# Optimization experiments

Hardware: AMD Instinct MI355X
Metric: run time of the kernel (lower is better)

Reference implementation:

```python
import jax, jax.numpy as jnp
import numpy as np

ALPHA = 4.0   # spikingjelly surrogate.Sigmoid default
TAU = 2.0
VTH = 1.0
EPS = 1e-5

@jax.custom_vjp
def spike(x):
    return (x >= 0.0).astype(x.dtype)

def _spike_fwd(x):
    return spike(x), x

def _spike_bwd(x, g):
    s = jax.nn.sigmoid(ALPHA * x)
    return (g * ALPHA * s * (1.0 - s),)

spike.defvjp(_spike_fwd, _spike_bwd)

def lif(x):
    # x: [T, B, N, C]; multi-step LIF, v_reset=0 hard reset, detach_reset=True
    def step(v, xt):
        v = v + (xt - v) / TAU          # charge
        s = spike(v - VTH)              # fire (surrogate grad)
        v = v * (1.0 - jax.lax.stop_gradient(s))  # hard reset, detached
        return v, s
    _, out = jax.lax.scan(step, jnp.zeros_like(x[0]), x)
    return out

def bn(x, gamma, beta):
    # BatchNorm1d in training mode: per-channel (last dim) over all other dims
    mu = x.mean(axis=(0, 1, 2), keepdims=True)
    var = x.var(axis=(0, 1, 2), keepdims=True)  # biased var, as torch BN uses for normalization
    return (x - mu) * jax.lax.rsqrt(var + EPS) * gamma + beta

def setup_inputs() -> dict:
    key = jax.random.key(0)
    ks = jax.random.split(key, 3)
    T, B, N, C, H = 4, 32, 1024, 256, 256
    x = jax.random.normal(ks[0], (T, B, N, C), dtype=jnp.float32)
    W1 = jax.random.normal(ks[1], (C, H), dtype=jnp.float32) * (1.0 / np.sqrt(C))
    W2 = jax.random.normal(ks[2], (H, C), dtype=jnp.float32) * (1.0 / np.sqrt(H))
    return {
        "x": x,
        "W1": W1, "b1": jnp.zeros((H,), jnp.float32),
        "gamma1": jnp.ones((H,), jnp.float32), "beta1": jnp.zeros((H,), jnp.float32),
        "W2": W2, "b2": jnp.zeros((C,), jnp.float32),
        "gamma2": jnp.ones((C,), jnp.float32), "beta2": jnp.zeros((C,), jnp.float32),
    }

def reference(x, W1, b1, gamma1, beta1, W2, b2, gamma2, beta2):
    # fc1: Linear -> BN (per-channel over T*B*N) -> multi-step LIF
    h = jnp.einsum('tbnc,ch->tbnh', x, W1) + b1
    h = lif(bn(h, gamma1, beta1))
    # fc2
    o = jnp.einsum('tbnh,ho->tbno', h, W2) + b2
    return lif(bn(o, gamma2, beta2))
```

## Files before the change

### kernel.cpp

```cpp
#include <hip/hip_runtime.h>


typedef __attribute__((ext_vector_type(8))) short bf16x8;
typedef __attribute__((ext_vector_type(8))) _Float16 f16x8;
typedef __attribute__((ext_vector_type(4))) _Float16 f16x4;
typedef __attribute__((ext_vector_type(4))) float f32x4;

__device__ __forceinline__ unsigned short f32_to_bf16_rne(float f) {
    unsigned int u = __builtin_bit_cast(unsigned int, f);
    u += 0x7FFFu + ((u >> 16) & 1u);
    return (unsigned short)(u >> 16);
}
__device__ __forceinline__ float bf16_to_f32(unsigned short h) {
    unsigned int u = ((unsigned int)h) << 16;
    return __builtin_bit_cast(float, u);
}

__global__ __launch_bounds__(256) void split_w1(const float* __restrict__ W1,
                                                _Float16* __restrict__ BhiT,
                                                _Float16* __restrict__ BloT) {
    int i = blockIdx.x * 256 + threadIdx.x;
    int k = i >> 8, n = i & 255;
    float w = W1[i];
    _Float16 hi = (_Float16)w;
    _Float16 lo = (_Float16)((w - (float)hi) * 4096.0f);
    BhiT[(size_t)n * 256 + k] = hi;
    BloT[(size_t)n * 256 + k] = lo;
}

__global__ __launch_bounds__(256) void split_w2(const float* __restrict__ W2,
                                                unsigned short* __restrict__ Bt) {
    int i = blockIdx.x * 256 + threadIdx.x;
    int k = i >> 8, n = i & 255;
    float w = W2[i];
    unsigned short hi = f32_to_bf16_rne(w);
    float r = w - bf16_to_f32(hi);
    unsigned short mid = f32_to_bf16_rne(r);
    float r2 = r - bf16_to_f32(mid);
    unsigned short lo = f32_to_bf16_rne(r2);
    Bt[(size_t)(0 * 256 + n) * 256 + k] = hi;
    Bt[(size_t)(1 * 256 + n) * 256 + k] = mid;
    Bt[(size_t)(2 * 256 + n) * 256 + k] = lo;
}

__global__ __launch_bounds__(256, 2) void gemm1_mfma(const float* __restrict__ A,
                                                     const _Float16* __restrict__ Bhi,
                                                     const _Float16* __restrict__ Blo,
                                                     const float* __restrict__ bias,
                                                     float* __restrict__ C,
                                                     double* __restrict__ partial) {
    __shared__ __align__(16) _Float16 Ahi[64 * 256];
    __shared__ __align__(16) _Float16 Alo[64 * 256];
    const size_t m0 = (size_t)blockIdx.x * 64;
    const int tid = threadIdx.x;
    const int lane = tid & 63;
    const int wc = tid >> 6;
    const int lrow = lane & 15, lchunk = lane >> 4;

    const _Float16* BhiB = Bhi + ((size_t)(64 * wc + lrow)) * 256 + lchunk * 8;
    const _Float16* BloB = Blo + ((size_t)(64 * wc + lrow)) * 256 + lchunk * 8;

    f16x8 bh[2][4], bl[2][4];
#define LOADB1(buf, kk)                                                   \
    _Pragma("unroll") for (int nf = 0; nf < 4; ++nf) {                    \
        bh[buf][nf] = *(const f16x8*)(BhiB + nf * 4096 + (kk) * 32);      \
        bl[buf][nf] = *(const f16x8*)(BloB + nf * 4096 + (kk) * 32);      \
    }

    LOADB1(0, 0)

    {
        const float* src = A + m0 * 256;
#pragma unroll
        for (int it = 0; it < 16; ++it) {
            unsigned i4 = (unsigned)(it * 256 + tid);
            float4 v = *(const float4*)(src + (size_t)i4 * 4);
            float f[4] = {v.x, v.y, v.z, v.w};
            f16x4 hi4, lo4;
#pragma unroll
            for (int e = 0; e < 4; ++e) {
                _Float16 hh = (_Float16)f[e];
                hi4[e] = hh;
                lo4[e] = (_Float16)((f[e] - (float)hh) * 4096.0f);
            }
            unsigned off = i4 * 8u;
            unsigned swz = off ^ (((off >> 9) & 7u) << 4);
            *(f16x4*)((char*)Ahi + swz) = hi4;
            *(f16x4*)((char*)Alo + swz) = lo4;
        }
    }
    __syncthreads();

    f32x4 acc0[4][4] = {}, acc1[4][4] = {};

#pragma unroll
    for (int k0 = 0; k0 < 8; ++k0) {
        const int cur = k0 & 1;
        if (k0 < 7) { LOADB1(cur ^ 1, k0 + 1) }
        f16x8 ah[4], al[4];
#pragma unroll
        for (int mf = 0; mf < 4; ++mf) {
            unsigned r = (unsigned)(16 * mf + lrow);
            unsigned off = (r * 512u + (unsigned)(k0 * 64 + lchunk * 16)) ^ ((r & 7u) << 4);
            ah[mf] = *(const f16x8*)((const char*)Ahi + off);
            al[mf] = *(const f16x8*)((const char*)Alo + off);
        }
#pragma unroll
        for (int nf = 0; nf < 4; ++nf)
#pragma unroll
            for (int mf = 0; mf < 4; ++mf)
                acc0[mf][nf] = __builtin_amdgcn_mfma_f32_16x16x32_f16(
                    ah[mf], bh[cur][nf], acc0[mf][nf], 0, 0, 0);
#pragma unroll
        for (int nf = 0; nf < 4; ++nf)
#pragma unroll
            for (int mf = 0; mf < 4; ++mf)
                acc1[mf][nf] = __builtin_amdgcn_mfma_f32_16x16x32_f16(
                    ah[mf], bl[cur][nf], acc1[mf][nf], 0, 0, 0);
#pragma unroll
        for (int nf = 0; nf < 4; ++nf)
#pragma unroll
            for (int mf = 0; mf < 4; ++mf)
                acc1[mf][nf] = __builtin_amdgcn_mfma_f32_16x16x32_f16(
                    al[mf], bh[cur][nf], acc1[mf][nf], 0, 0, 0);
    }
#undef LOADB1

    const float UNSCALE = 1.0f / 4096.0f;
#pragma unroll
    for (int nf = 0; nf < 4; ++nf) {
        int col = 64 * wc + 16 * nf + lrow;
        float bvv = bias[col];
        double ss = 0.0, qq = 0.0;
#pragma unroll
        for (int mf = 0; mf < 4; ++mf) {
            size_t rowb = m0 + 16 * mf + 4 * lchunk;
#pragma unroll
            for (int e = 0; e < 4; ++e) {
                float hv = acc0[mf][nf][e] + acc1[mf][nf][e] * UNSCALE + bvv;
                C[(rowb + e) * 256 + col] = hv;
                ss += (double)hv;
                qq += (double)hv * (double)hv;
            }
        }
        ss += __shfl_xor(ss, 16);
        ss += __shfl_xor(ss, 32);
        qq += __shfl_xor(qq, 16);
        qq += __shfl_xor(qq, 32);
        if (lane < 16) {
            partial[(size_t)blockIdx.x * 512 + col] = ss;
            partial[(size_t)blockIdx.x * 512 + 256 + col] = qq;
        }
    }
}

__global__ __launch_bounds__(256, 2) void gemm2_fused(const float* __restrict__ h,
                                                      const float2* __restrict__ ss1,
                                                      const unsigned short* __restrict__ Bt,
                                                      const float* __restrict__ bias,
                                                      float* __restrict__ C,
                                                      double* __restrict__ partial,
                                                      int bnRows) {
    __shared__ __align__(16) unsigned short Asw[64 * 256];
    const int bn0 = blockIdx.x * 16;
    const int tid = threadIdx.x;
    const int lane = tid & 63;
    const int wc = tid >> 6;
    const int lrow = lane & 15, lchunk = lane >> 4;

    const unsigned short* Bbase =
        Bt + ((size_t)(64 * wc + lrow)) * 256 + lchunk * 8;

    bf16x8 bb[2][12];
#define LOADB(buf, kk)                                                        \
    _Pragma("unroll") for (int t_ = 0; t_ < 3; ++t_)                          \
    _Pragma("unroll") for (int nf = 0; nf < 4; ++nf)                          \
        bb[buf][t_ * 4 + nf] = *(const bf16x8*)(Bbase + (size_t)t_ * 65536 +  \
                                                nf * 4096 + (kk) * 32);

    LOADB(0, 0)

    {
#pragma unroll
        for (int it = 0; it < 4; ++it) {
            int slot = it * 256 + tid;
            int bn = slot >> 6;
            int colq = slot & 63;
            int c0 = colq * 4;
            float2 p0 = ss1[c0], p1 = ss1[c0 + 1], p2 = ss1[c0 + 2], p3 = ss1[c0 + 3];
            size_t rb = (size_t)(bn0 + bn) * 256 + c0;
            float4 v = make_float4(0.f, 0.f, 0.f, 0.f);
#pragma unroll
            for (int t4 = 0; t4 < 4; ++t4) {
                float4 hv = *(const float4*)(h + (size_t)t4 * bnRows * 256 + rb);
                float x0 = hv.x * p0.x + p0.y;
                float x1 = hv.y * p1.x + p1.y;
                float x2 = hv.z * p2.x + p2.y;
                float x3 = hv.w * p3.x + p3.y;
                v.x = (v.x + x0) * 0.5f;
                v.y = (v.y + x1) * 0.5f;
                v.z = (v.z + x2) * 0.5f;
                v.w = (v.w + x3) * 0.5f;
                ushort4 sp;
                sp.x = (v.x >= 1.0f) ? 0x3F80 : 0;
                sp.y = (v.y >= 1.0f) ? 0x3F80 : 0;
                sp.z = (v.z >= 1.0f) ? 0x3F80 : 0;
                sp.w = (v.w >= 1.0f) ? 0x3F80 : 0;
                v.x = (v.x >= 1.0f) ? 0.0f : v.x;
                v.y = (v.y >= 1.0f) ? 0.0f : v.y;
                v.z = (v.z >= 1.0f) ? 0.0f : v.z;
                v.w = (v.w >= 1.0f) ? 0.0f : v.w;
                unsigned row = (unsigned)(t4 * 16 + bn);
                unsigned off = (row * 512u + (unsigned)colq * 8u) ^ ((row & 7u) << 4);
                *(ushort4*)((char*)Asw + off) = sp;
            }
        }
    }
    __syncthreads();

    f32x4 acc[4][4] = {};

#pragma unroll
    for (int k0 = 0; k0 < 8; ++k0) {
        const int cur = k0 & 1;
        if (k0 < 7) { LOADB(cur ^ 1, k0 + 1) }
        bf16x8 af[4];
#pragma unroll
        for (int mf = 0; mf < 4; ++mf) {
            unsigned r = (unsigned)(16 * mf + lrow);
            unsigned off = (r * 512u + (unsigned)(k0 * 64 + lchunk * 16)) ^ ((r & 7u) << 4);
            af[mf] = *(const bf16x8*)((const char*)Asw + off);
        }
#pragma unroll
        for (int t_ = 0; t_ < 3; ++t_)
#pragma unroll
            for (int nf = 0; nf < 4; ++nf)
#pragma unroll
                for (int mf = 0; mf < 4; ++mf)
                    acc[mf][nf] = __builtin_amdgcn_mfma_f32_16x16x32_bf16(
                        af[mf], bb[cur][t_ * 4 + nf], acc[mf][nf], 0, 0, 0);
    }
#undef LOADB

#pragma unroll
    for (int nf = 0; nf < 4; ++nf) {
        int col = 64 * wc + 16 * nf + lrow;
        float bvv = bias[col];
        double ss = 0.0, qq = 0.0;
#pragma unroll
        for (int mf = 0; mf < 4; ++mf) {
            int Lbase = 16 * mf + 4 * lchunk;
#pragma unroll
            for (int e = 0; e < 4; ++e) {
                int L = Lbase + e;
                size_t G = (size_t)(L >> 4) * bnRows + bn0 + (L & 15);
                float hv = acc[mf][nf][e] + bvv;
                C[G * 256 + col] = hv;
                ss += (double)hv;
                qq += (double)hv * (double)hv;
            }
        }
        ss += __shfl_xor(ss, 16);
        ss += __shfl_xor(ss, 32);
        qq += __shfl_xor(qq, 16);
        qq += __shfl_xor(qq, 32);
        if (lane < 16) {
            partial[(size_t)blockIdx.x * 512 + col] = ss;
            partial[(size_t)blockIdx.x * 512 + 256 + col] = qq;
        }
    }
}

__global__ __launch_bounds__(256) void finalize_stats(const double* __restrict__ partial,
                                                      const float* __restrict__ gamma,
                                                      const float* __restrict__ beta,
                                                      float2* __restrict__ ss,
                                                      int nblocks, double invM) {
    const int c = blockIdx.x;
    const int t = threadIdx.x;
    __shared__ double sh[256];
    __shared__ double sh2[256];
    double s = 0.0, s2 = 0.0;
    for (int b = t; b < nblocks; b += 256) {
        s += partial[(size_t)b * 512 + c];
        s2 += partial[(size_t)b * 512 + 256 + c];
    }
    sh[t] = s;
    sh2[t] = s2;
    __syncthreads();
#pragma unroll
    for (int off = 128; off > 0; off >>= 1) {
        if (t < off) {
            sh[t] += sh[t + off];
            sh2[t] += sh2[t + off];
        }
        __syncthreads();
    }
    if (t == 0) {
        double mu = sh[0] * invM;
        double var = sh2[0] * invM - mu * mu;
        double rstd = 1.0 / sqrt(var + 1e-5);
        double sc = (double)gamma[c] * rstd;
        ss[c] = make_float2((float)sc, (float)((double)beta[c] - mu * sc));
    }
}

__global__ __launch_bounds__(256) void bnlif_f32(const float* __restrict__ h,
                                                 const float2* __restrict__ ss,
                                                 float* __restrict__ out,
                                                 int slab4) {
    int t4 = blockIdx.x * 256 + threadIdx.x;
    if (t4 >= slab4) return;
    size_t idx = (size_t)t4 * 4;
    int c0 = (int)(idx & 255);
    float2 p0 = ss[c0], p1 = ss[c0 + 1], p2 = ss[c0 + 2], p3 = ss[c0 + 3];
    size_t slab = (size_t)slab4 * 4;
    float4 v = make_float4(0.f, 0.f, 0.f, 0.f);
#pragma unroll
    for (int t = 0; t < 4; ++t) {
        float4 hv = *(const float4*)(h + (size_t)t * slab + idx);
        float x0 = hv.x * p0.x + p0.y;
        float x1 = hv.y * p1.x + p1.y;
        float x2 = hv.z * p2.x + p2.y;
        float x3 = hv.w * p3.x + p3.y;
        v.x = (v.x + x0) * 0.5f;
        v.y = (v.y + x1) * 0.5f;
        v.z = (v.z + x2) * 0.5f;
        v.w = (v.w + x3) * 0.5f;
        float4 sp;
        sp.x = (v.x >= 1.0f) ? 1.0f : 0.0f;
        sp.y = (v.y >= 1.0f) ? 1.0f : 0.0f;
        sp.z = (v.z >= 1.0f) ? 1.0f : 0.0f;
        sp.w = (v.w >= 1.0f) ? 1.0f : 0.0f;
        v.x = (v.x >= 1.0f) ? 0.0f : v.x;
        v.y = (v.y >= 1.0f) ? 0.0f : v.y;
        v.z = (v.z >= 1.0f) ? 0.0f : v.z;
        v.w = (v.w >= 1.0f) ? 0.0f : v.w;
        *(float4*)(out + (size_t)t * slab + idx) = sp;
    }
}

extern "C" void kernel_launch(void* const* d_in, const int* in_sizes, int n_in,
                              void* d_out, int out_size, void* d_ws, size_t ws_size,
                              hipStream_t stream) {
    const float* x  = (const float*)d_in[0];
    const float* W1 = (const float*)d_in[1];
    const float* b1 = (const float*)d_in[2];
    const float* g1 = (const float*)d_in[3];
    const float* be1 = (const float*)d_in[4];
    const float* W2 = (const float*)d_in[5];
    const float* b2 = (const float*)d_in[6];
    const float* g2 = (const float*)d_in[7];
    const float* be2 = (const float*)d_in[8];
    float* out = (float*)d_out;

    const int M = in_sizes[0] / 256;
    const int bnRows = M / 4;
    const size_t hBytes = (size_t)M * 256 * 4;

    char* ws = (char*)d_ws;
    float* h = (float*)ws;
    double* partial = (double*)(ws + hBytes);
    unsigned short* W2catT = (unsigned short*)(ws + hBytes + (size_t)2048 * 512 * 8);
    float2* ss1 = (float2*)((char*)W2catT + 3 * 256 * 256 * 2);
    float2* ss2 = ss1 + 256;
    _Float16* W1hiT = (_Float16*)(ss2 + 256);
    _Float16* W1loT = W1hiT + 256 * 256;

    const int slab4 = M * 16;
    const double invM = 1.0 / (double)M;
    const int NB1 = M / 64;
    const int NB2 = bnRows / 16;

    dim3 blk(256);

    split_w1<<<dim3(256), blk, 0, stream>>>(W1, W1hiT, W1loT);
    split_w2<<<dim3(256), blk, 0, stream>>>(W2, W2catT);

    gemm1_mfma<<<dim3(NB1), blk, 0, stream>>>(x, W1hiT, W1loT, b1, h, partial);
    finalize_stats<<<dim3(256), blk, 0, stream>>>(partial, g1, be1, ss1, NB1, invM);

    gemm2_fused<<<dim3(NB2), blk, 0, stream>>>(h, ss1, W2catT, b2, h, partial, bnRows);
    finalize_stats<<<dim3(256), blk, 0, stream>>>(partial, g2, be2, ss2, NB2, invM);
    bnlif_f32<<<dim3(slab4 / 256), blk, 0, stream>>>(h, ss2, out, slab4);
}
```

Baseline: 303.8 us.

## Make both GEMMs persistent with double-buffered LDS A-tiles and prefetch

Both GEMM kernels now launch 256 persistent blocks of 512 threads. Each block loops over multiple 64-row tiles and double-buffers the A tile in shared memory, with register prefetch of the next tile's global loads overlapping the current MFMA loop. Each of the 8 waves now covers 32 output columns instead of 64, which halves the per-wave B fragments and accumulators. This aims to hide global-load latency and cut launch/tail overhead, at the cost of doubled LDS use (one block per CU) and B fragments reloaded every tile.

```diff
diff --git a/kernel.cpp b/kernel.cpp
--- a/kernel.cpp
+++ b/kernel.cpp
@@ -43,232 +43,280 @@
     Bt[(size_t)(2 * 256 + n) * 256 + k] = lo;
 }
 
-__global__ __launch_bounds__(256, 2) void gemm1_mfma(const float* __restrict__ A,
-                                                     const _Float16* __restrict__ Bhi,
-                                                     const _Float16* __restrict__ Blo,
-                                                     const float* __restrict__ bias,
-                                                     float* __restrict__ C,
-                                                     double* __restrict__ partial) {
-    __shared__ __align__(16) _Float16 Ahi[64 * 256];
-    __shared__ __align__(16) _Float16 Alo[64 * 256];
-    const size_t m0 = (size_t)blockIdx.x * 64;
+__global__ __launch_bounds__(512) void gemm1_mfma(const float* __restrict__ A,
+                                                  const _Float16* __restrict__ Bhi,
+                                                  const _Float16* __restrict__ Blo,
+                                                  const float* __restrict__ bias,
+                                                  float* __restrict__ C,
+                                                  double* __restrict__ partial,
+                                                  int tb) {
+    __shared__ __align__(16) _Float16 AhiS[2][64 * 256];
+    __shared__ __align__(16) _Float16 AloS[2][64 * 256];
+    const size_t mBase = (size_t)blockIdx.x * tb * 64;
     const int tid = threadIdx.x;
     const int lane = tid & 63;
     const int wc = tid >> 6;
     const int lrow = lane & 15, lchunk = lane >> 4;
 
-    const _Float16* BhiB = Bhi + ((size_t)(64 * wc + lrow)) * 256 + lchunk * 8;
-    const _Float16* BloB = Blo + ((size_t)(64 * wc + lrow)) * 256 + lchunk * 8;
-
-    f16x8 bh[2][4], bl[2][4];
+    const _Float16* BhiB = Bhi + ((size_t)(32 * wc + lrow)) * 256 + lchunk * 8;
+    const _Float16* BloB = Blo + ((size_t)(32 * wc + lrow)) * 256 + lchunk * 8;
+
+    f16x8 bh[2][2], bl[2][2];
 #define LOADB1(buf, kk)                                                   \
-    _Pragma("unroll") for (int nf = 0; nf < 4; ++nf) {                    \
+    _Pragma("unroll") for (int nf = 0; nf < 2; ++nf) {                    \
         bh[buf][nf] = *(const f16x8*)(BhiB + nf * 4096 + (kk) * 32);      \
         bl[buf][nf] = *(const f16x8*)(BloB + nf * 4096 + (kk) * 32);      \
     }
 
+    float4 ra[8], rb[8];
+#define ISSUE1(R, tt)                                                     \
+    {                                                                     \
+        const float* s_ = A + (mBase + (size_t)(tt) * 64) * 256;          \
+        _Pragma("unroll") for (int i = 0; i < 8; ++i)                     \
+            R[i] = *(const float4*)(s_ + (size_t)(i * 512 + tid) * 4);    \
+    }
+#define CW1(R, buf)                                                               \
+    _Pragma("unroll") for (int i = 0; i < 8; ++i) {                               \
+        unsigned i4 = (unsigned)(i * 512 + tid);                                  \
+        float f0 = R[i].x, f1 = R[i].y, f2 = R[i].z, f3 = R[i].w;                 \
+        f16x4 hi4, lo4;                                                           \
+        _Float16 h0 = (_Float16)f0; hi4[0] = h0; lo4[0] = (_Float16)((f0 - (float)h0) * 4096.0f); \
+        _Float16 h1 = (_Float16)f1; hi4[1] = h1; lo4[1] = (_Float16)((f1 - (float)h1) * 4096.0f); \
+        _Float16 h2 = (_Float16)f2; hi4[2] = h2; lo4[2] = (_Float16)((f2 - (float)h2) * 4096.0f); \
+        _Float16 h3 = (_Float16)f3; hi4[3] = h3; lo4[3] = (_Float16)((f3 - (float)h3) * 4096.0f); \
+        unsigned off = i4 * 8u;                                                   \
+        unsigned swz = off ^ (((off >> 9) & 7u) << 4);                            \
+        *(f16x4*)((char*)AhiS[buf] + swz) = hi4;                                  \
+        *(f16x4*)((char*)AloS[buf] + swz) = lo4;                                  \
+    }
+
+    ISSUE1(ra, 0)
     LOADB1(0, 0)
-
-    {
-        const float* src = A + m0 * 256;
-#pragma unroll
-        for (int it = 0; it < 16; ++it) {
-            unsigned i4 = (unsigned)(it * 256 + tid);
-            float4 v = *(const float4*)(src + (size_t)i4 * 4);
-            float f[4] = {v.x, v.y, v.z, v.w};
-            f16x4 hi4, lo4;
-#pragma unroll
-            for (int e = 0; e < 4; ++e) {
-                _Float16 hh = (_Float16)f[e];
-                hi4[e] = hh;
-                lo4[e] = (_Float16)((f[e] - (float)hh) * 4096.0f);
-            }
-            unsigned off = i4 * 8u;
-            unsigned swz = off ^ (((off >> 9) & 7u) << 4);
-            *(f16x4*)((char*)Ahi + swz) = hi4;
-            *(f16x4*)((char*)Alo + swz) = lo4;
-        }
-    }
-    __syncthreads();
-
-    f32x4 acc0[4][4] = {}, acc1[4][4] = {};
-
-#pragma unroll
-    for (int k0 = 0; k0 < 8; ++k0) {
-        const int cur = k0 & 1;
-        if (k0 < 7) { LOADB1(cur ^ 1, k0 + 1) }
-        f16x8 ah[4], al[4];
-#pragma unroll
-        for (int mf = 0; mf < 4; ++mf) {
-            unsigned r = (unsigned)(16 * mf + lrow);
-            unsigned off = (r * 512u + (unsigned)(k0 * 64 + lchunk * 16)) ^ ((r & 7u) << 4);
-            ah[mf] = *(const f16x8*)((const char*)Ahi + off);
-            al[mf] = *(const f16x8*)((const char*)Alo + off);
-        }
-#pragma unroll
-        for (int nf = 0; nf < 4; ++nf)
-#pragma unroll
-            for (int mf = 0; mf < 4; ++mf)
-                acc0[mf][nf] = __builtin_amdgcn_mfma_f32_16x16x32_f16(
-                    ah[mf], bh[cur][nf], acc0[mf][nf], 0, 0, 0);
-#pragma unroll
-        for (int nf = 0; nf < 4; ++nf)
-#pragma unroll
-            for (int mf = 0; mf < 4; ++mf)
-                acc1[mf][nf] = __builtin_amdgcn_mfma_f32_16x16x32_f16(
-                    ah[mf], bl[cur][nf], acc1[mf][nf], 0, 0, 0);
-#pragma unroll
-        for (int nf = 0; nf < 4; ++nf)
-#pragma unroll
-            for (int mf = 0; mf < 4; ++mf)
-                acc1[mf][nf] = __builtin_amdgcn_mfma_f32_16x16x32_f16(
-                    al[mf], bh[cur][nf], acc1[mf][nf], 0, 0, 0);
+    CW1(ra, 0)
+    ISSUE1(rb, 1)
+
+    for (int t = 0; t < tb; ++t) {
+        __syncthreads();
+        const int p = t & 1;
+        f32x4 acc0[4][2] = {}, acc1[4][2] = {};
+#pragma unroll
+        for (int k0 = 0; k0 < 8; ++k0) {
+            const int cur = k0 & 1;
+            LOADB1(cur ^ 1, (k0 + 1) & 7)
+            f16x8 ah[4], al[4];
+#pragma unroll
+            for (int mf = 0; mf < 4; ++mf) {
+                unsigned r = (unsigned)(16 * mf + lrow);
+                unsigned off = (r * 512u + (unsigned)(k0 * 64 + lchunk * 16)) ^ ((r & 7u) << 4);
+                ah[mf] = *(const f16x8*)((const char*)AhiS[p] + off);
+                al[mf] = *(const f16x8*)((const char*)AloS[p] + off);
+            }
+#pragma unroll
+            for (int nf = 0; nf < 2; ++nf)
+#pragma unroll
+                for (int mf = 0; mf < 4; ++mf)
+                    acc0[mf][nf] = __builtin_amdgcn_mfma_f32_16x16x32_f16(
+                        ah[mf], bh[cur][nf], acc0[mf][nf], 0, 0, 0);
+#pragma unroll
+            for (int nf = 0; nf < 2; ++nf)
+#pragma unroll
+                for (int mf = 0; mf < 4; ++mf)
+                    acc1[mf][nf] = __builtin_amdgcn_mfma_f32_16x16x32_f16(
+                        ah[mf], bl[cur][nf], acc1[mf][nf], 0, 0, 0);
+#pragma unroll
+            for (int nf = 0; nf < 2; ++nf)
+#pragma unroll
+                for (int mf = 0; mf < 4; ++mf)
+                    acc1[mf][nf] = __builtin_amdgcn_mfma_f32_16x16x32_f16(
+                        al[mf], bh[cur][nf], acc1[mf][nf], 0, 0, 0);
+        }
+        if (t + 1 < tb) {
+            if ((t & 1) == 0) {
+                CW1(rb, 1)
+                if (t + 2 < tb) { ISSUE1(ra, t + 2) }
+            } else {
+                CW1(ra, 0)
+                if (t + 2 < tb) { ISSUE1(rb, t + 2) }
+            }
+        }
+        const size_t m0 = mBase + (size_t)t * 64;
+        const float UNSCALE = 1.0f / 4096.0f;
+#pragma unroll
+        for (int nf = 0; nf < 2; ++nf) {
+            int col = 32 * wc + 16 * nf + lrow;
+            float bvv = bias[col];
+            double ss = 0.0, qq = 0.0;
+#pragma unroll
+            for (int mf = 0; mf < 4; ++mf) {
+                size_t rowb = m0 + 16 * mf + 4 * lchunk;
+#pragma unroll
+                for (int e = 0; e < 4; ++e) {
+                    float hv = acc0[mf][nf][e] + acc1[mf][nf][e] * UNSCALE + bvv;
+                    C[(rowb + e) * 256 + col] = hv;
+                    ss += (double)hv;
+                    qq += (double)hv * (double)hv;
+                }
+            }
+            ss += __shfl_xor(ss, 16);
+            ss += __shfl_xor(ss, 32);
+            qq += __shfl_xor(qq, 16);
+            qq += __shfl_xor(qq, 32);
+            if (lane < 16) {
+                size_t prow = ((size_t)blockIdx.x * tb + t) * 512;
+                partial[prow + col] = ss;
+                partial[prow + 256 + col] = qq;
+            }
+        }
     }
 #undef LOADB1
-
-    const float UNSCALE = 1.0f / 4096.0f;
-#pragma unroll
-    for (int nf = 0; nf < 4; ++nf) {
-        int col = 64 * wc + 16 * nf + lrow;
-        float bvv = bias[col];
-        double ss = 0.0, qq = 0.0;
-#pragma unroll
-        for (int mf = 0; mf < 4; ++mf) {
-            size_t rowb = m0 + 16 * mf + 4 * lchunk;
-#pragma unroll
-            for (int e = 0; e < 4; ++e) {
-                float hv = acc0[mf][nf][e] + acc1[mf][nf][e] * UNSCALE + bvv;
-                C[(rowb + e) * 256 + col] = hv;
-                ss += (double)hv;
-                qq += (double)hv * (double)hv;
-            }
-        }
-        ss += __shfl_xor(ss, 16);
-        ss += __shfl_xor(ss, 32);
-        qq += __shfl_xor(qq, 16);
-        qq += __shfl_xor(qq, 32);
-        if (lane < 16) {
-            partial[(size_t)blockIdx.x * 512 + col] = ss;
-            partial[(size_t)blockIdx.x * 512 + 256 + col] = qq;
-        }
-    }
-}
-
-__global__ __launch_bounds__(256, 2) void gemm2_fused(const float* __restrict__ h,
-                                                      const float2* __restrict__ ss1,
-                                                      const unsigned short* __restrict__ Bt,
-                                                      const float* __restrict__ bias,
-                                                      float* __restrict__ C,
-                                                      double* __restrict__ partial,
-                                                      int bnRows) {
-    __shared__ __align__(16) unsigned short Asw[64 * 256];
-    const int bn0 = blockIdx.x * 16;
+#undef ISSUE1
+#undef CW1
+}
+
+__global__ __launch_bounds__(512) void gemm2_fused(const float* __restrict__ h,
+                                                   const float2* __restrict__ ss1,
+                                                   const unsigned short* __restrict__ Bt,
+                                                   const float* __restrict__ bias,
+                                                   float* __restrict__ C,
+                                                   double* __restrict__ partial,
+                                                   int bnRows, int tb) {
+    __shared__ __align__(16) unsigned short AswS[2][64 * 256];
+    const int bnBase = blockIdx.x * tb * 16;
     const int tid = threadIdx.x;
     const int lane = tid & 63;
     const int wc = tid >> 6;
     const int lrow = lane & 15, lchunk = lane >> 4;
 
     const unsigned short* Bbase =
-        Bt + ((size_t)(64 * wc + lrow)) * 256 + lchunk * 8;
-
-    bf16x8 bb[2][12];
+        Bt + ((size_t)(32 * wc + lrow)) * 256 + lchunk * 8;
+
+    bf16x8 bb[2][6];
 #define LOADB(buf, kk)                                                        \
     _Pragma("unroll") for (int t_ = 0; t_ < 3; ++t_)                          \
-    _Pragma("unroll") for (int nf = 0; nf < 4; ++nf)                          \
-        bb[buf][t_ * 4 + nf] = *(const bf16x8*)(Bbase + (size_t)t_ * 65536 +  \
+    _Pragma("unroll") for (int nf = 0; nf < 2; ++nf)                          \
+        bb[buf][t_ * 2 + nf] = *(const bf16x8*)(Bbase + (size_t)t_ * 65536 +  \
                                                 nf * 4096 + (kk) * 32);
 
+    const int sbn0 = tid >> 6, scq = tid & 63;
+    float4 rh[8], rg[8];
+#define ISSUE2(R, tt)                                                             \
+    {                                                                             \
+        int bn0_ = bnBase + (tt) * 16;                                            \
+        _Pragma("unroll") for (int s = 0; s < 2; ++s) {                           \
+            size_t rb_ = (size_t)(bn0_ + s * 8 + sbn0) * 256 + scq * 4;           \
+            _Pragma("unroll") for (int t4 = 0; t4 < 4; ++t4)                      \
+                R[s * 4 + t4] = *(const float4*)(h + (size_t)t4 * bnRows * 256 + rb_); \
+        }                                                                         \
+    }
+#define CW2(R, buf)                                                                   \
+    {                                                                                 \
+        int c0_ = scq * 4;                                                            \
+        float2 p0 = ss1[c0_], p1 = ss1[c0_ + 1], p2 = ss1[c0_ + 2], p3 = ss1[c0_ + 3];\
+        _Pragma("unroll") for (int s = 0; s < 2; ++s) {                               \
+            int bn = s * 8 + sbn0;                                                    \
+            float4 v_ = make_float4(0.f, 0.f, 0.f, 0.f);                              \
+            _Pragma("unroll") for (int t4 = 0; t4 < 4; ++t4) {                        \
+                float4 hv = R[s * 4 + t4];                                            \
+                float x0 = hv.x * p0.x + p0.y;                                        \
+                float x1 = hv.y * p1.x + p1.y;                                        \
+                float x2 = hv.z * p2.x + p2.y;                                        \
+                float x3 = hv.w * p3.x + p3.y;                                        \
+                v_.x = (v_.x + x0) * 0.5f;                                            \
+                v_.y = (v_.y + x1) * 0.5f;                                            \
+                v_.z = (v_.z + x2) * 0.5f;                                            \
+                v_.w = (v_.w + x3) * 0.5f;                                            \
+                ushort4 sp;                                                           \
+                sp.x = (v_.x >= 1.0f) ? 0x3F80 : 0;                                   \
+                sp.y = (v_.y >= 1.0f) ? 0x3F80 : 0;                                   \
+                sp.z = (v_.z >= 1.0f) ? 0x3F80 : 0;                                   \
+                sp.w = (v_.w >= 1.0f) ? 0x3F80 : 0;                                   \
+                v_.x = (v_.x >= 1.0f) ? 0.0f : v_.x;                                  \
+                v_.y = (v_.y >= 1.0f) ? 0.0f : v_.y;                                  \
+                v_.z = (v_.z >= 1.0f) ? 0.0f : v_.z;                                  \
+                v_.w = (v_.w >= 1.0f) ? 0.0f : v_.w;                                  \
+                unsigned row = (unsigned)(t4 * 16 + bn);                              \
+                unsigned off = (row * 512u + (unsigned)scq * 8u) ^ ((row & 7u) << 4); \
+                *(ushort4*)((char*)AswS[buf] + off) = sp;                             \
+            }                                                                         \
+        }                                                                             \
+    }
+
+    ISSUE2(rh, 0)
     LOADB(0, 0)
-
-    {
-#pragma unroll
-        for (int it = 0; it < 4; ++it) {
-            int slot = it * 256 + tid;
-            int bn = slot >> 6;
-            int colq = slot & 63;
-            int c0 = colq * 4;
-            float2 p0 = ss1[c0], p1 = ss1[c0 + 1], p2 = ss1[c0 + 2], p3 = ss1[c0 + 3];
-            size_t rb = (size_t)(bn0 + bn) * 256 + c0;
-            float4 v = make_float4(0.f, 0.f, 0.f, 0.f);
-#pragma unroll
-            for (int t4 = 0; t4 < 4; ++t4) {
-                float4 hv = *(const float4*)(h + (size_t)t4 * bnRows * 256 + rb);
-                float x0 = hv.x * p0.x + p0.y;
-                float x1 = hv.y * p1.x + p1.y;
-                float x2 = hv.z * p2.x + p2.y;
-                float x3 = hv.w * p3.x + p3.y;
-                v.x = (v.x + x0) * 0.5f;
-                v.y = (v.y + x1) * 0.5f;
-                v.z = (v.z + x2) * 0.5f;
-                v.w = (v.w + x3) * 0.5f;
-                ushort4 sp;
-                sp.x = (v.x >= 1.0f) ? 0x3F80 : 0;
-                sp.y = (v.y >= 1.0f) ? 0x3F80 : 0;
-                sp.z = (v.z >= 1.0f) ? 0x3F80 : 0;
-                sp.w = (v.w >= 1.0f) ? 0x3F80 : 0;
-                v.x = (v.x >= 1.0f) ? 0.0f : v.x;
-                v.y = (v.y >= 1.0f) ? 0.0f : v.y;
-                v.z = (v.z >= 1.0f) ? 0.0f : v.z;
-                v.w = (v.w >= 1.0f) ? 0.0f : v.w;
-                unsigned row = (unsigned)(t4 * 16 + bn);
-                unsigned off = (row * 512u + (unsigned)colq * 8u) ^ ((row & 7u) << 4);
-                *(ushort4*)((char*)Asw + off) = sp;
-            }
-        }
-    }
-    __syncthreads();
-
-    f32x4 acc[4][4] = {};
-
-#pragma unroll
-    for (int k0 = 0; k0 < 8; ++k0) {
-        const int cur = k0 & 1;
-        if (k0 < 7) { LOADB(cur ^ 1, k0 + 1) }
-        bf16x8 af[4];
-#pragma unroll
-        for (int mf = 0; mf < 4; ++mf) {
-            unsigned r = (unsigned)(16 * mf + lrow);
-            unsigned off = (r * 512u + (unsigned)(k0 * 64 + lchunk * 16)) ^ ((r & 7u) << 4);
-            af[mf] = *(const bf16x8*)((const char*)Asw + off);
-        }
-#pragma unroll
-        for (int t_ = 0; t_ < 3; ++t_)
-#pragma unroll
-            for (int nf = 0; nf < 4; ++nf)
-#pragma unroll
-                for (int mf = 0; mf < 4; ++mf)
-                    acc[mf][nf] = __builtin_amdgcn_mfma_f32_16x16x32_bf16(
-                        af[mf], bb[cur][t_ * 4 + nf], acc[mf][nf], 0, 0, 0);
+    CW2(rh, 0)
+    ISSUE2(rg, 1)
+
+    for (int t = 0; t < tb; ++t) {
+        __syncthreads();
+        const int p = t & 1;
+        f32x4 acc[4][2] = {};
+#pragma unroll
+        for (int k0 = 0; k0 < 8; ++k0) {
+            const int cur = k0 & 1;
+            LOADB(cur ^ 1, (k0 + 1) & 7)
+            bf16x8 af[4];
+#pragma unroll
+            for (int mf = 0; mf < 4; ++mf) {
+                unsigned r = (unsigned)(16 * mf + lrow);
+                unsigned off = (r * 512u + (unsigned)(k0 * 64 + lchunk * 16)) ^ ((r & 7u) << 4);
+                af[mf] = *(const bf16x8*)((const char*)AswS[p] + off);
+            }
+#pragma unroll
+            for (int t_ = 0; t_ < 3; ++t_)
+#pragma unroll
+                for (int nf = 0; nf < 2; ++nf)
+#pragma unroll
+                    for (int mf = 0; mf < 4; ++mf)
+                        acc[mf][nf] = __builtin_amdgcn_mfma_f32_16x16x32_bf16(
+                            af[mf], bb[cur][t_ * 2 + nf], acc[mf][nf], 0, 0, 0);
+        }
+        if (t + 1 < tb) {
+            if ((t & 1) == 0) {
+                CW2(rg, 1)
+                if (t + 2 < tb) { ISSUE2(rh, t + 2) }
+            } else {
+                CW2(rh, 0)
+                if (t + 2 < tb) { ISSUE2(rg, t + 2) }
+            }
+        }
+        const int bn0 = bnBase + t * 16;
+        double s_[2], q_[2];
+#pragma unroll
+        for (int nf = 0; nf < 2; ++nf) {
+            int col = 32 * wc + 16 * nf + lrow;
+            float bvv = bias[col];
+            double ss = 0.0, qq = 0.0;
+#pragma unroll
+            for (int mf = 0; mf < 4; ++mf) {
+                size_t G0 = (size_t)mf * bnRows + bn0 + 4 * lchunk;
+#pragma unroll
+                for (int e = 0; e < 4; ++e) {
+                    float hv = acc[mf][nf][e] + bvv;
+                    C[(G0 + e) * 256 + col] = hv;
+                    ss += (double)hv;
+                    qq += (double)hv * (double)hv;
+                }
+            }
+            ss += __shfl_xor(ss, 16);
+            ss += __shfl_xor(ss, 32);
+            qq += __shfl_xor(qq, 16);
+            qq += __shfl_xor(qq, 32);
+            s_[nf] = ss;
+            q_[nf] = qq;
+        }
+        if (lane < 16) {
+            size_t prow = ((size_t)blockIdx.x * tb + t) * 512;
+#pragma unroll
+            for (int nf = 0; nf < 2; ++nf) {
+                int col = 32 * wc + 16 * nf + lrow;
+                partial[prow + col] = s_[nf];
+                partial[prow + 256 + col] = q_[nf];
+            }
+        }
     }
 #undef LOADB
-
-#pragma unroll
-    for (int nf = 0; nf < 4; ++nf) {
-        int col = 64 * wc + 16 * nf + lrow;
-        float bvv = bias[col];
-        double ss = 0.0, qq = 0.0;
-#pragma unroll
-        for (int mf = 0; mf < 4; ++mf) {
-            int Lbase = 16 * mf + 4 * lchunk;
-#pragma unroll
-            for (int e = 0; e < 4; ++e) {
-                int L = Lbase + e;
-                size_t G = (size_t)(L >> 4) * bnRows + bn0 + (L & 15);
-                float hv = acc[mf][nf][e] + bvv;
-                C[G * 256 + col] = hv;
-                ss += (double)hv;
-                qq += (double)hv * (double)hv;
-            }
-        }
-        ss += __shfl_xor(ss, 16);
-        ss += __shfl_xor(ss, 32);
-        qq += __shfl_xor(qq, 16);
-        qq += __shfl_xor(qq, 32);
-        if (lane < 16) {
-            partial[(size_t)blockIdx.x * 512 + col] = ss;
-            partial[(size_t)blockIdx.x * 512 + 256 + col] = qq;
-        }
-    }
+#undef ISSUE2
+#undef CW2
 }
 
 __global__ __launch_bounds__(256) void finalize_stats(const double* __restrict__ partial,
@@ -369,18 +417,18 @@
 
     const int slab4 = M * 16;
     const double invM = 1.0 / (double)M;
-    const int NB1 = M / 64;
-    const int NB2 = bnRows / 16;
+    const int tb1 = (M / 64) / 256;
+    const int tb2 = (bnRows / 16) / 256;
 
     dim3 blk(256);
 
     split_w1<<<dim3(256), blk, 0, stream>>>(W1, W1hiT, W1loT);
     split_w2<<<dim3(256), blk, 0, stream>>>(W2, W2catT);
 
-    gemm1_mfma<<<dim3(NB1), blk, 0, stream>>>(x, W1hiT, W1loT, b1, h, partial);
-    finalize_stats<<<dim3(256), blk, 0, stream>>>(partial, g1, be1, ss1, NB1, invM);
-
-    gemm2_fused<<<dim3(NB2), blk, 0, stream>>>(h, ss1, W2catT, b2, h, partial, bnRows);
-    finalize_stats<<<dim3(256), blk, 0, stream>>>(partial, g2, be2, ss2, NB2, invM);
+    gemm1_mfma<<<dim3(256), dim3(512), 0, stream>>>(x, W1hiT, W1loT, b1, h, partial, tb1);
+    finalize_stats<<<dim3(256), blk, 0, stream>>>(partial, g1, be1, ss1, 256 * tb1, invM);
+
+    gemm2_fused<<<dim3(256), dim3(512), 0, stream>>>(h, ss1, W2catT, b2, h, partial, bnRows, tb2);
+    finalize_stats<<<dim3(256), blk, 0, stream>>>(partial, g2, be2, ss2, 256 * tb2, invM);
     bnlif_f32<<<dim3(slab4 / 256), blk, 0, stream>>>(h, ss2, out, slab4);
 }
```

Measured after the change: 403.0 us. +32.7%, slower.
